# Kernel tuning notes

Hardware: AMD Instinct MI355X
Metric: run time of the kernel (lower is better)

## Reference

```python
import jax, jax.numpy as jnp
import numpy as np

V, E, D, B, C = 100000, 256, 128, 8192, 10  # vocab, embedding_size, context_size, batch, window


def setup_inputs() -> dict:
    key = jax.random.key(0)
    ks = jax.random.split(key, 11)
    s = 0.02
    return {
        "x": jax.random.randint(ks[0], (B,), 0, V),
        "context": jax.random.randint(ks[1], (B, C), 0, V),
        "W_emb": jax.random.normal(ks[2], (V, E), jnp.float32) * s,
        "M_w": jax.random.normal(ks[3], (D, E), jnp.float32) * s,
        "M_b": jnp.zeros((D,), jnp.float32),
        "U_w": jax.random.normal(ks[4], (D, 2 * D), jnp.float32) * s,
        "U_b": jnp.zeros((D,), jnp.float32),
        "W_w": jax.random.normal(ks[5], (D, 2 * D), jnp.float32) * s,
        "W_b": jnp.zeros((D,), jnp.float32),
        "prior_mus": jax.random.normal(ks[6], (V, D), jnp.float32) * s,
        # covariance diagonal must be positive for a valid Gaussian (torch would
        # Cholesky-fail otherwise); sample in [0.1, 1.0)
        "prior_sigmas": jax.random.uniform(ks[7], (V, D), jnp.float32, 0.1, 1.0),
    }


def reference(x, context, W_emb, M_w, M_b, U_w, U_b, W_w, W_b, prior_mus, prior_sigmas):
    emb_x = W_emb[x]                       # [B, E]
    emb_c = W_emb[context]                 # [B, C, E]
    Rw = emb_x @ M_w.T + M_b               # [B, D]  (repeated over C slots below)
    Rc = jnp.einsum('bce,de->bcd', emb_c, M_w) + M_b  # [B, C, D]
    RwC = jnp.broadcast_to(Rw[:, None, :], Rc.shape)   # repeat(len(context), 1)
    h = jax.nn.relu(jnp.concatenate([RwC, Rc], axis=-1)).sum(axis=1)  # [B, 2D]
    mu = h @ U_w.T + U_b                   # posterior mean  [B, D]
    sigma = jax.nn.softplus(h @ W_w.T + W_b)  # posterior cov diag [B, D]
    m0 = prior_mus[x]                      # prior mean      [B, D]
    s0 = prior_sigmas[x]                   # prior cov diag  [B, D]
    # closed-form KL(N(m0, diag(s0)) || N(mu, diag(sigma)))
    d = jnp.float32(D)
    kl = 0.5 * ((s0 / sigma).sum(-1)
                + ((mu - m0) ** 2 / sigma).sum(-1)
                - d
                + jnp.log(sigma).sum(-1) - jnp.log(s0).sum(-1))
    return kl  # [B]
```

## Files before the change

kernel.cpp:

```cpp
#include <hip/hip_runtime.h>
#include <hip/hip_bf16.h>
#include <math.h>


#define CTXN  10
#define EDIM  256
#define DDIM  128
#define WS_M   0
#define WS_UW  32768
#define WS_H   98304

typedef short bf16x8 __attribute__((ext_vector_type(8)));
typedef float f32x4  __attribute__((ext_vector_type(4)));

__device__ __forceinline__ uint2 cvt4(float4 v) {
    union { __hip_bfloat162 h2; unsigned u; } a, b;
    a.h2 = __float22bfloat162_rn(make_float2(v.x, v.y));
    b.h2 = __float22bfloat162_rn(make_float2(v.z, v.w));
    return make_uint2(a.u, b.u);
}

__device__ __forceinline__ float softplusf(float v) {
    return fmaxf(v, 0.0f) + log1pf(expf(-fabsf(v)));
}

__global__ __launch_bounds__(256) void k_cvt(
    const float* __restrict__ M_w, const float* __restrict__ U_w,
    const float* __restrict__ W_w, unsigned short* __restrict__ ws)
{
    int which = blockIdx.x >> 5;
    int i = ((blockIdx.x & 31) << 8) | threadIdx.x;
    const float* src = (which == 0) ? M_w : (which == 1) ? U_w : W_w;
    float4 v = ((const float4*)src)[i];
    *(uint2*)&ws[which * 32768 + i * 4] = cvt4(v);
}

#define BT1   8
#define ROWS1 88
#define LP    72
#define ACH   (96 * LP)

__device__ __forceinline__ void load_A8(const float* __restrict__ W_emb,
                                        const int* idx_s, int k0f4, int tid,
                                        float4* sreg) {
#pragma unroll
    for (int s = 0; s < 3; ++s) {
        int it = tid + 512 * s;
        if (it < ROWS1 * 16) {
            int r = it >> 4, q = it & 15;
            sreg[s] = ((const float4*)W_emb)[(size_t)idx_s[r] * 64 + k0f4 + q];
        }
    }
}
__device__ __forceinline__ void write_A8(unsigned short* A, int tid,
                                         const float4* sreg) {
#pragma unroll
    for (int s = 0; s < 3; ++s) {
        int it = tid + 512 * s;
        if (it < ROWS1 * 16) {
            int r = it >> 4, q = it & 15;
            *(uint2*)&A[r * LP + 4 * q] = cvt4(sreg[s]);
        }
    }
}

__global__ __launch_bounds__(512, 4) void bsg_h(
    const int* __restrict__ x, const int* __restrict__ ctx,
    const float* __restrict__ W_emb, const float* __restrict__ M_b,
    const unsigned short* __restrict__ wsr, unsigned short* __restrict__ hws)
{
    __shared__ unsigned short A_s[2 * ACH];
    __shared__ int idx_s[ROWS1];

    const int tid  = threadIdx.x;
    const int b0   = blockIdx.x * BT1;
    const int w    = tid >> 6;
    const int lane = tid & 63;
    const int l15  = lane & 15;
    const int lg   = lane >> 4;

    if (tid < ROWS1) {
        int c = tid >> 3, b = b0 + (tid & 7);
        idx_s[tid] = (c == 0) ? x[b] : ctx[b * CTXN + (c - 1)];
    }
    __syncthreads();

    float4 sreg[3];
    load_A8(W_emb, idx_s, 0, tid, sreg);
    write_A8(A_s, tid, sreg);

    const unsigned short* Mb_bf = wsr + WS_M;
    const int mrow = 16 * w + l15;
    f32x4 acc[6] = {};

#pragma unroll
    for (int ch = 0; ch < 4; ++ch) {
        if (ch < 3) load_A8(W_emb, idx_s, (ch + 1) * 16, tid, sreg);
        __syncthreads();
        bf16x8 m0 = *(const bf16x8*)&Mb_bf[mrow * 256 + 64 * ch + 8 * lg];
        bf16x8 m1 = *(const bf16x8*)&Mb_bf[mrow * 256 + 64 * ch + 32 + 8 * lg];
        const unsigned short* Ab = A_s + (ch & 1) * ACH;
#pragma unroll
        for (int mt = 0; mt < 6; ++mt) {
            bf16x8 a0 = *(const bf16x8*)&Ab[(16 * mt + l15) * LP + 8 * lg];
            bf16x8 a1 = *(const bf16x8*)&Ab[(16 * mt + l15) * LP + 32 + 8 * lg];
            acc[mt] = __builtin_amdgcn_mfma_f32_16x16x32_bf16(a0, m0, acc[mt], 0, 0, 0);
            acc[mt] = __builtin_amdgcn_mfma_f32_16x16x32_bf16(a1, m1, acc[mt], 0, 0, 0);
        }
        if (ch < 3) write_A8(A_s + ((ch + 1) & 1) * ACH, tid, sreg);
    }

    const int dg = 16 * w + l15;
    const float mb = M_b[dg];
    float p1[4] = {0, 0, 0, 0}, p2[4] = {0, 0, 0, 0};
#pragma unroll
    for (int mt = 0; mt < 6; ++mt) {
#pragma unroll
        for (int q = 0; q < 4; ++q) {
            float r = fmaxf(acc[mt][q] + mb, 0.0f);
            if (lg < 2) { if (mt == 0) p1[q] = r; else p2[q] += r; }
            else        { if (mt < 5)  p2[q] += r; }
        }
    }
#pragma unroll
    for (int q = 0; q < 4; ++q) {
        float other = __shfl_xor(p2[q], 32);
        if (lg < 2) {
            int b = 4 * lg + q;
            __hip_bfloat16 t1 = __float2bfloat16(10.0f * p1[q]);
            __hip_bfloat16 t2 = __float2bfloat16(p2[q] + other);
            hws[(size_t)(b0 + b) * 256 + dg]       = *(unsigned short*)&t1;
            hws[(size_t)(b0 + b) * 256 + 128 + dg] = *(unsigned short*)&t2;
        }
    }
}

#define BT2  32
#define HLP  264

__global__ __launch_bounds__(512, 4) void bsg_kl(
    const int* __restrict__ x, const float* __restrict__ U_b,
    const float* __restrict__ W_b, const float* __restrict__ pmu,
    const float* __restrict__ psg, const unsigned short* __restrict__ wsr,
    float* __restrict__ out)
{
    __shared__ unsigned short H_s[BT2 * HLP];
    __shared__ int   xs[BT2];
    __shared__ float P_s[BT2 * 8];

    const int tid  = threadIdx.x;
    const int b0   = blockIdx.x * BT2;
    const int w    = tid >> 6;
    const int lane = tid & 63;
    const int l15  = lane & 15;
    const int lg   = lane >> 4;

    if (tid < BT2) xs[tid] = x[b0 + tid];
    const unsigned short* hws = wsr + WS_H;
#pragma unroll
    for (int s = 0; s < 2; ++s) {
        int it = tid + 512 * s;
        int r = it >> 5, q = it & 31;
        *(uint4*)&H_s[r * HLP + 8 * q] =
            *(const uint4*)&hws[(size_t)(b0 + r) * 256 + 8 * q];
    }
    __syncthreads();

    const unsigned short* UWb = wsr + WS_UW;
    const int nrow = 16 * w + l15;
    f32x4 acc2[2][2] = {};
#pragma unroll
    for (int ks = 0; ks < 8; ++ks) {
        bf16x8 bu = *(const bf16x8*)&UWb[nrow * 256 + 32 * ks + 8 * lg];
        bf16x8 bw = *(const bf16x8*)&UWb[(128 + nrow) * 256 + 32 * ks + 8 * lg];
#pragma unroll
        for (int mt = 0; mt < 2; ++mt) {
            bf16x8 hf = *(const bf16x8*)&H_s[(16 * mt + l15) * HLP + 32 * ks + 8 * lg];
            acc2[mt][0] = __builtin_amdgcn_mfma_f32_16x16x32_bf16(hf, bu, acc2[mt][0], 0, 0, 0);
            acc2[mt][1] = __builtin_amdgcn_mfma_f32_16x16x32_bf16(hf, bw, acc2[mt][1], 0, 0, 0);
        }
    }

    const int d = 16 * w + l15;
    const float ub = U_b[d], wb = W_b[d];
#pragma unroll
    for (int mt = 0; mt < 2; ++mt) {
#pragma unroll
        for (int q = 0; q < 4; ++q) {
            int rb = 16 * mt + 4 * lg + q;
            int xb = xs[rb];
            float mu = acc2[mt][0][q] + ub;
            float sg = softplusf(acc2[mt][1][q] + wb);
            float m0 = pmu[(size_t)xb * DDIM + d];
            float s0 = psg[(size_t)xb * DDIM + d];
            float dm = mu - m0;
            float p  = s0 / sg + dm * dm / sg + logf(sg) - logf(s0);
            p += __shfl_xor(p, 1);
            p += __shfl_xor(p, 2);
            p += __shfl_xor(p, 4);
            p += __shfl_xor(p, 8);
            if (l15 == 0) P_s[rb * 8 + w] = p;
        }
    }
    __syncthreads();
    if (tid < BT2) {
        float s = 0.0f;
#pragma unroll
        for (int k = 0; k < 8; ++k) s += P_s[tid * 8 + k];
        out[b0 + tid] = 0.5f * (s - (float)DDIM);
    }
}

extern "C" void kernel_launch(void* const* d_in, const int* in_sizes, int n_in,
                              void* d_out, int out_size, void* d_ws, size_t ws_size,
                              hipStream_t stream) {
    const int*   x     = (const int*)  d_in[0];
    const int*   ctx   = (const int*)  d_in[1];
    const float* W_emb = (const float*)d_in[2];
    const float* M_w   = (const float*)d_in[3];
    const float* M_b   = (const float*)d_in[4];
    const float* U_w   = (const float*)d_in[5];
    const float* U_b   = (const float*)d_in[6];
    const float* W_w   = (const float*)d_in[7];
    const float* W_b   = (const float*)d_in[8];
    const float* pmu   = (const float*)d_in[9];
    const float* psg   = (const float*)d_in[10];
    float* out = (float*)d_out;
    unsigned short* ws = (unsigned short*)d_ws;

    k_cvt<<<dim3(96), dim3(256), 0, stream>>>(M_w, U_w, W_w, ws);
    bsg_h<<<dim3(8192 / BT1), dim3(512), 0, stream>>>(x, ctx, W_emb, M_b,
                                                      ws, ws + WS_H);
    bsg_kl<<<dim3(8192 / BT2), dim3(512), 0, stream>>>(x, U_b, W_b, pmu, psg,
                                                       ws, out);
}
```

Baseline: 44.60 us.

## Fuse hidden-state and KL kernels into one, keeping h in shared memory

Merges the h-computation kernel and the KL kernel into a single kernel that processes 8 batch rows per block. The hidden vector h stays in LDS instead of being written to and read back from a global workspace, and the prior mean and sigma loads are issued early, before the epilogue, to hide their latency. This removes one launch and the h round trip through global memory. In exchange, the second GEMM now runs on only 8 rows per block using 16-row MFMA tiles, so half of its work is wasted, and the U and W weights are re-read by four times as many blocks.

```diff
diff --git a/kernel.cpp b/kernel.cpp
--- a/kernel.cpp
+++ b/kernel.cpp
@@ -4,11 +4,15 @@
 
 
 #define CTXN  10
-#define EDIM  256
 #define DDIM  128
 #define WS_M   0
 #define WS_UW  32768
-#define WS_H   98304
+
+#define BT    8
+#define ROWS  88
+#define LP    72
+#define ACH   (96 * LP)
+#define HLP   264
 
 typedef short bf16x8 __attribute__((ext_vector_type(8)));
 typedef float f32x4  __attribute__((ext_vector_type(4)));
@@ -35,18 +39,13 @@
     *(uint2*)&ws[which * 32768 + i * 4] = cvt4(v);
 }
 
-#define BT1   8
-#define ROWS1 88
-#define LP    72
-#define ACH   (96 * LP)
-
 __device__ __forceinline__ void load_A8(const float* __restrict__ W_emb,
                                         const int* idx_s, int k0f4, int tid,
                                         float4* sreg) {
 #pragma unroll
     for (int s = 0; s < 3; ++s) {
         int it = tid + 512 * s;
-        if (it < ROWS1 * 16) {
+        if (it < ROWS * 16) {
             int r = it >> 4, q = it & 15;
             sreg[s] = ((const float4*)W_emb)[(size_t)idx_s[r] * 64 + k0f4 + q];
         }
@@ -57,29 +56,33 @@
 #pragma unroll
     for (int s = 0; s < 3; ++s) {
         int it = tid + 512 * s;
-        if (it < ROWS1 * 16) {
+        if (it < ROWS * 16) {
             int r = it >> 4, q = it & 15;
             *(uint2*)&A[r * LP + 4 * q] = cvt4(sreg[s]);
         }
     }
 }
 
-__global__ __launch_bounds__(512, 4) void bsg_h(
+__global__ __launch_bounds__(512, 4) void bsg_fused(
     const int* __restrict__ x, const int* __restrict__ ctx,
     const float* __restrict__ W_emb, const float* __restrict__ M_b,
-    const unsigned short* __restrict__ wsr, unsigned short* __restrict__ hws)
+    const float* __restrict__ U_b,   const float* __restrict__ W_b,
+    const float* __restrict__ pmu,   const float* __restrict__ psg,
+    const unsigned short* __restrict__ wsr, float* __restrict__ out)
 {
     __shared__ unsigned short A_s[2 * ACH];
-    __shared__ int idx_s[ROWS1];
+    __shared__ unsigned short H_s[8 * HLP];
+    __shared__ int   idx_s[ROWS];
+    __shared__ float P_s[BT * 8];
 
     const int tid  = threadIdx.x;
-    const int b0   = blockIdx.x * BT1;
+    const int b0   = blockIdx.x * BT;
     const int w    = tid >> 6;
     const int lane = tid & 63;
     const int l15  = lane & 15;
     const int lg   = lane >> 4;
 
-    if (tid < ROWS1) {
+    if (tid < ROWS) {
         int c = tid >> 3, b = b0 + (tid & 7);
         idx_s[tid] = (c == 0) ? x[b] : ctx[b * CTXN + (c - 1)];
     }
@@ -110,6 +113,14 @@
         if (ch < 3) write_A8(A_s + ((ch + 1) & 1) * ACH, tid, sreg);
     }
 
+    float pm[4], ps[4];
+#pragma unroll
+    for (int q = 0; q < 4; ++q) {
+        int xb = idx_s[(4 * lg + q) & 7];
+        pm[q] = pmu[(size_t)xb * DDIM + 16 * w + l15];
+        ps[q] = psg[(size_t)xb * DDIM + 16 * w + l15];
+    }
+
     const int dg = 16 * w + l15;
     const float mb = M_b[dg];
     float p1[4] = {0, 0, 0, 0}, p2[4] = {0, 0, 0, 0};
@@ -129,81 +140,40 @@
             int b = 4 * lg + q;
             __hip_bfloat16 t1 = __float2bfloat16(10.0f * p1[q]);
             __hip_bfloat16 t2 = __float2bfloat16(p2[q] + other);
-            hws[(size_t)(b0 + b) * 256 + dg]       = *(unsigned short*)&t1;
-            hws[(size_t)(b0 + b) * 256 + 128 + dg] = *(unsigned short*)&t2;
-        }
-    }
-}
-
-#define BT2  32
-#define HLP  264
-
-__global__ __launch_bounds__(512, 4) void bsg_kl(
-    const int* __restrict__ x, const float* __restrict__ U_b,
-    const float* __restrict__ W_b, const float* __restrict__ pmu,
-    const float* __restrict__ psg, const unsigned short* __restrict__ wsr,
-    float* __restrict__ out)
-{
-    __shared__ unsigned short H_s[BT2 * HLP];
-    __shared__ int   xs[BT2];
-    __shared__ float P_s[BT2 * 8];
-
-    const int tid  = threadIdx.x;
-    const int b0   = blockIdx.x * BT2;
-    const int w    = tid >> 6;
-    const int lane = tid & 63;
-    const int l15  = lane & 15;
-    const int lg   = lane >> 4;
-
-    if (tid < BT2) xs[tid] = x[b0 + tid];
-    const unsigned short* hws = wsr + WS_H;
-#pragma unroll
-    for (int s = 0; s < 2; ++s) {
-        int it = tid + 512 * s;
-        int r = it >> 5, q = it & 31;
-        *(uint4*)&H_s[r * HLP + 8 * q] =
-            *(const uint4*)&hws[(size_t)(b0 + r) * 256 + 8 * q];
+            H_s[b * HLP + dg]       = *(unsigned short*)&t1;
+            H_s[b * HLP + 128 + dg] = *(unsigned short*)&t2;
+        }
     }
     __syncthreads();
 
     const unsigned short* UWb = wsr + WS_UW;
     const int nrow = 16 * w + l15;
-    f32x4 acc2[2][2] = {};
+    f32x4 acc2[2] = {};
 #pragma unroll
     for (int ks = 0; ks < 8; ++ks) {
+        bf16x8 hf = *(const bf16x8*)&H_s[(l15 & 7) * HLP + 32 * ks + 8 * lg];
         bf16x8 bu = *(const bf16x8*)&UWb[nrow * 256 + 32 * ks + 8 * lg];
         bf16x8 bw = *(const bf16x8*)&UWb[(128 + nrow) * 256 + 32 * ks + 8 * lg];
-#pragma unroll
-        for (int mt = 0; mt < 2; ++mt) {
-            bf16x8 hf = *(const bf16x8*)&H_s[(16 * mt + l15) * HLP + 32 * ks + 8 * lg];
-            acc2[mt][0] = __builtin_amdgcn_mfma_f32_16x16x32_bf16(hf, bu, acc2[mt][0], 0, 0, 0);
-            acc2[mt][1] = __builtin_amdgcn_mfma_f32_16x16x32_bf16(hf, bw, acc2[mt][1], 0, 0, 0);
-        }
-    }
-
-    const int d = 16 * w + l15;
-    const float ub = U_b[d], wb = W_b[d];
-#pragma unroll
-    for (int mt = 0; mt < 2; ++mt) {
-#pragma unroll
-        for (int q = 0; q < 4; ++q) {
-            int rb = 16 * mt + 4 * lg + q;
-            int xb = xs[rb];
-            float mu = acc2[mt][0][q] + ub;
-            float sg = softplusf(acc2[mt][1][q] + wb);
-            float m0 = pmu[(size_t)xb * DDIM + d];
-            float s0 = psg[(size_t)xb * DDIM + d];
-            float dm = mu - m0;
-            float p  = s0 / sg + dm * dm / sg + logf(sg) - logf(s0);
-            p += __shfl_xor(p, 1);
-            p += __shfl_xor(p, 2);
-            p += __shfl_xor(p, 4);
-            p += __shfl_xor(p, 8);
-            if (l15 == 0) P_s[rb * 8 + w] = p;
-        }
+        acc2[0] = __builtin_amdgcn_mfma_f32_16x16x32_bf16(hf, bu, acc2[0], 0, 0, 0);
+        acc2[1] = __builtin_amdgcn_mfma_f32_16x16x32_bf16(hf, bw, acc2[1], 0, 0, 0);
+    }
+
+    const float ub = U_b[16 * w + l15];
+    const float wb = W_b[16 * w + l15];
+#pragma unroll
+    for (int q = 0; q < 4; ++q) {
+        float mu = acc2[0][q] + ub;
+        float sg = softplusf(acc2[1][q] + wb);
+        float dm = mu - pm[q];
+        float p  = ps[q] / sg + dm * dm / sg + logf(sg) - logf(ps[q]);
+        p += __shfl_xor(p, 1);
+        p += __shfl_xor(p, 2);
+        p += __shfl_xor(p, 4);
+        p += __shfl_xor(p, 8);
+        if (l15 == 0 && lg < 2) P_s[(4 * lg + q) * 8 + w] = p;
     }
     __syncthreads();
-    if (tid < BT2) {
+    if (tid < BT) {
         float s = 0.0f;
 #pragma unroll
         for (int k = 0; k < 8; ++k) s += P_s[tid * 8 + k];
@@ -229,8 +199,6 @@
     unsigned short* ws = (unsigned short*)d_ws;
 
     k_cvt<<<dim3(96), dim3(256), 0, stream>>>(M_w, U_w, W_w, ws);
-    bsg_h<<<dim3(8192 / BT1), dim3(512), 0, stream>>>(x, ctx, W_emb, M_b,
-                                                      ws, ws + WS_H);
-    bsg_kl<<<dim3(8192 / BT2), dim3(512), 0, stream>>>(x, U_b, W_b, pmu, psg,
-                                                       ws, out);
-}
+    bsg_fused<<<dim3(8192 / BT), dim3(512), 0, stream>>>(
+        x, ctx, W_emb, M_b, U_b, W_b, pmu, psg, ws, out);
+}
```

New measurement: 49.34 us. 1.11x slower.

## Prefetch all embedding chunks and weights upfront; halve KL batch tile

Applied to the files above, without the earlier changes.

In the h kernel, all four K-chunks of the gathered embedding rows are now loaded into registers at once (12 float4 per thread), and the M weights are held in registers before the first barrier. This exposes all gather latency together instead of interleaving one chunk per iteration. In the KL kernel, the batch tile drops from 32 to 16 rows so twice as many blocks run, and the prior mu/sigma gathers are issued at kernel start to overlap with the H load and MFMA. The cost is much higher register pressure, which may reduce occupancy, plus reloading the U/W weights across more blocks.

```diff
diff --git a/kernel.cpp b/kernel.cpp
--- a/kernel.cpp
+++ b/kernel.cpp
@@ -4,7 +4,6 @@
 
 
 #define CTXN  10
-#define EDIM  256
 #define DDIM  128
 #define WS_M   0
 #define WS_UW  32768
@@ -40,30 +39,6 @@
 #define LP    72
 #define ACH   (96 * LP)
 
-__device__ __forceinline__ void load_A8(const float* __restrict__ W_emb,
-                                        const int* idx_s, int k0f4, int tid,
-                                        float4* sreg) {
-#pragma unroll
-    for (int s = 0; s < 3; ++s) {
-        int it = tid + 512 * s;
-        if (it < ROWS1 * 16) {
-            int r = it >> 4, q = it & 15;
-            sreg[s] = ((const float4*)W_emb)[(size_t)idx_s[r] * 64 + k0f4 + q];
-        }
-    }
-}
-__device__ __forceinline__ void write_A8(unsigned short* A, int tid,
-                                         const float4* sreg) {
-#pragma unroll
-    for (int s = 0; s < 3; ++s) {
-        int it = tid + 512 * s;
-        if (it < ROWS1 * 16) {
-            int r = it >> 4, q = it & 15;
-            *(uint2*)&A[r * LP + 4 * q] = cvt4(sreg[s]);
-        }
-    }
-}
-
 __global__ __launch_bounds__(512, 4) void bsg_h(
     const int* __restrict__ x, const int* __restrict__ ctx,
     const float* __restrict__ W_emb, const float* __restrict__ M_b,
@@ -83,31 +58,50 @@
         int c = tid >> 3, b = b0 + (tid & 7);
         idx_s[tid] = (c == 0) ? x[b] : ctx[b * CTXN + (c - 1)];
     }
-    __syncthreads();
-
-    float4 sreg[3];
-    load_A8(W_emb, idx_s, 0, tid, sreg);
-    write_A8(A_s, tid, sreg);
 
     const unsigned short* Mb_bf = wsr + WS_M;
     const int mrow = 16 * w + l15;
+    bf16x8 mreg[8];
+#pragma unroll
+    for (int kk = 0; kk < 8; ++kk)
+        mreg[kk] = *(const bf16x8*)&Mb_bf[mrow * 256 + 32 * kk + 8 * lg];
+
+    __syncthreads();
+
+    float4 rr[12];
+#pragma unroll
+    for (int ch = 0; ch < 4; ++ch)
+#pragma unroll
+        for (int s = 0; s < 3; ++s) {
+            int it = tid + 512 * s;
+            if (it < ROWS1 * 16) {
+                int r = it >> 4, q = it & 15;
+                rr[ch * 3 + s] =
+                    ((const float4*)W_emb)[(size_t)idx_s[r] * 64 + ch * 16 + q];
+            }
+        }
+
     f32x4 acc[6] = {};
-
 #pragma unroll
     for (int ch = 0; ch < 4; ++ch) {
-        if (ch < 3) load_A8(W_emb, idx_s, (ch + 1) * 16, tid, sreg);
+        unsigned short* Ab = A_s + (ch & 1) * ACH;
+#pragma unroll
+        for (int s = 0; s < 3; ++s) {
+            int it = tid + 512 * s;
+            if (it < ROWS1 * 16) {
+                int r = it >> 4, q = it & 15;
+                *(uint2*)&Ab[r * LP + 4 * q] = cvt4(rr[ch * 3 + s]);
+            }
+        }
         __syncthreads();
-        bf16x8 m0 = *(const bf16x8*)&Mb_bf[mrow * 256 + 64 * ch + 8 * lg];
-        bf16x8 m1 = *(const bf16x8*)&Mb_bf[mrow * 256 + 64 * ch + 32 + 8 * lg];
-        const unsigned short* Ab = A_s + (ch & 1) * ACH;
+        const unsigned short* Abr = A_s + (ch & 1) * ACH;
 #pragma unroll
         for (int mt = 0; mt < 6; ++mt) {
-            bf16x8 a0 = *(const bf16x8*)&Ab[(16 * mt + l15) * LP + 8 * lg];
-            bf16x8 a1 = *(const bf16x8*)&Ab[(16 * mt + l15) * LP + 32 + 8 * lg];
-            acc[mt] = __builtin_amdgcn_mfma_f32_16x16x32_bf16(a0, m0, acc[mt], 0, 0, 0);
-            acc[mt] = __builtin_amdgcn_mfma_f32_16x16x32_bf16(a1, m1, acc[mt], 0, 0, 0);
-        }
-        if (ch < 3) write_A8(A_s + ((ch + 1) & 1) * ACH, tid, sreg);
+            bf16x8 a0 = *(const bf16x8*)&Abr[(16 * mt + l15) * LP + 8 * lg];
+            bf16x8 a1 = *(const bf16x8*)&Abr[(16 * mt + l15) * LP + 32 + 8 * lg];
+            acc[mt] = __builtin_amdgcn_mfma_f32_16x16x32_bf16(a0, mreg[2 * ch],     acc[mt], 0, 0, 0);
+            acc[mt] = __builtin_amdgcn_mfma_f32_16x16x32_bf16(a1, mreg[2 * ch + 1], acc[mt], 0, 0, 0);
+        }
     }
 
     const int dg = 16 * w + l15;
@@ -135,7 +129,7 @@
     }
 }
 
-#define BT2  32
+#define BT2  16
 #define HLP  264
 
 __global__ __launch_bounds__(512, 4) void bsg_kl(
@@ -145,7 +139,6 @@
     float* __restrict__ out)
 {
     __shared__ unsigned short H_s[BT2 * HLP];
-    __shared__ int   xs[BT2];
     __shared__ float P_s[BT2 * 8];
 
     const int tid  = threadIdx.x;
@@ -154,53 +147,48 @@
     const int lane = tid & 63;
     const int l15  = lane & 15;
     const int lg   = lane >> 4;
-
-    if (tid < BT2) xs[tid] = x[b0 + tid];
+    const int d    = 16 * w + l15;
+
+    float pm[4], ps[4];
+#pragma unroll
+    for (int q = 0; q < 4; ++q) {
+        int xb = x[b0 + 4 * lg + q];
+        pm[q] = pmu[(size_t)xb * DDIM + d];
+        ps[q] = psg[(size_t)xb * DDIM + d];
+    }
+
     const unsigned short* hws = wsr + WS_H;
-#pragma unroll
-    for (int s = 0; s < 2; ++s) {
-        int it = tid + 512 * s;
-        int r = it >> 5, q = it & 31;
+    {
+        int r = tid >> 5, q = tid & 31;
         *(uint4*)&H_s[r * HLP + 8 * q] =
             *(const uint4*)&hws[(size_t)(b0 + r) * 256 + 8 * q];
     }
     __syncthreads();
 
     const unsigned short* UWb = wsr + WS_UW;
-    const int nrow = 16 * w + l15;
-    f32x4 acc2[2][2] = {};
+    f32x4 acc2[2] = {};
 #pragma unroll
     for (int ks = 0; ks < 8; ++ks) {
-        bf16x8 bu = *(const bf16x8*)&UWb[nrow * 256 + 32 * ks + 8 * lg];
-        bf16x8 bw = *(const bf16x8*)&UWb[(128 + nrow) * 256 + 32 * ks + 8 * lg];
-#pragma unroll
-        for (int mt = 0; mt < 2; ++mt) {
-            bf16x8 hf = *(const bf16x8*)&H_s[(16 * mt + l15) * HLP + 32 * ks + 8 * lg];
-            acc2[mt][0] = __builtin_amdgcn_mfma_f32_16x16x32_bf16(hf, bu, acc2[mt][0], 0, 0, 0);
-            acc2[mt][1] = __builtin_amdgcn_mfma_f32_16x16x32_bf16(hf, bw, acc2[mt][1], 0, 0, 0);
-        }
-    }
-
-    const int d = 16 * w + l15;
+        bf16x8 hf = *(const bf16x8*)&H_s[l15 * HLP + 32 * ks + 8 * lg];
+        bf16x8 bu = *(const bf16x8*)&UWb[d * 256 + 32 * ks + 8 * lg];
+        bf16x8 bw = *(const bf16x8*)&UWb[(128 + d) * 256 + 32 * ks + 8 * lg];
+        acc2[0] = __builtin_amdgcn_mfma_f32_16x16x32_bf16(hf, bu, acc2[0], 0, 0, 0);
+        acc2[1] = __builtin_amdgcn_mfma_f32_16x16x32_bf16(hf, bw, acc2[1], 0, 0, 0);
+    }
+
     const float ub = U_b[d], wb = W_b[d];
 #pragma unroll
-    for (int mt = 0; mt < 2; ++mt) {
-#pragma unroll
-        for (int q = 0; q < 4; ++q) {
-            int rb = 16 * mt + 4 * lg + q;
-            int xb = xs[rb];
-            float mu = acc2[mt][0][q] + ub;
-            float sg = softplusf(acc2[mt][1][q] + wb);
-            float m0 = pmu[(size_t)xb * DDIM + d];
-            float s0 = psg[(size_t)xb * DDIM + d];
-            float dm = mu - m0;
-            float p  = s0 / sg + dm * dm / sg + logf(sg) - logf(s0);
-            p += __shfl_xor(p, 1);
-            p += __shfl_xor(p, 2);
-            p += __shfl_xor(p, 4);
-            p += __shfl_xor(p, 8);
-            if (l15 == 0) P_s[rb * 8 + w] = p;
-        }
+    for (int q = 0; q < 4; ++q) {
+        int rb = 4 * lg + q;
+        float mu = acc2[0][q] + ub;
+        float sg = softplusf(acc2[1][q] + wb);
+        float dm = mu - pm[q];
+        float p  = ps[q] / sg + dm * dm / sg + logf(sg) - logf(ps[q]);
+        p += __shfl_xor(p, 1);
+        p += __shfl_xor(p, 2);
+        p += __shfl_xor(p, 4);
+        p += __shfl_xor(p, 8);
+        if (l15 == 0) P_s[rb * 8 + w] = p;
     }
     __syncthreads();
     if (tid < BT2) {
```

New measurement: 47.91 us. 1.07x slower.
